# Performance work log

Hardware: AMD Instinct MI355X
Metric: run time of the kernel (lower is better)

The kernel has to match this reference:

```python
import jax, jax.numpy as jnp
import numpy as np

# Dimensions inferred from VSSBlockOneWay(hidden_dim=256, ssm_d_state=64, forward_type='m0_noz')
B_, L_, D_ = 8, 2048, 256      # batch, seq_len, d_model
DIN, N_, P_ = 512, 64, 64      # d_inner = 2*d_model, d_state, head_dim
H_ = DIN // P_                 # n_heads = 8


def _ln(x, w, b, eps=1e-5):
    m = x.mean(-1, keepdims=True)
    v = ((x - m) ** 2).mean(-1, keepdims=True)
    return (x - m) * jax.lax.rsqrt(v + eps) * w + b


def setup_inputs() -> dict:
    key = jax.random.key(0)
    ks = jax.random.split(key, 8)
    s = lambda k, shape, sc: jax.random.normal(k, shape, jnp.float32) * sc
    return dict(
        src=jax.random.normal(ks[0], (B_, L_, D_), jnp.float32),
        ln_w=jnp.ones((D_,), jnp.float32), ln_b=jnp.zeros((D_,), jnp.float32),
        W_in=s(ks[1], (D_, DIN), 0.02),
        conv_w=s(ks[2], (DIN, 1, 3), 0.1),            # depthwise conv1d kernel
        conv_b=jnp.zeros((DIN,), jnp.float32),
        W_xproj=s(ks[3], (DIN, H_ + 2 * N_), 0.02),   # -> (dt | B | C)
        dt_bias=s(ks[4], (H_,), 0.1),
        A_log=jnp.log(jnp.arange(1, H_ + 1, dtype=jnp.float32)),  # Mamba2 A-init
        Ds=jnp.ones((H_,), jnp.float32),
        oln_w=jnp.ones((DIN,), jnp.float32), oln_b=jnp.zeros((DIN,), jnp.float32),
        W_out=s(ks[5], (DIN, D_), 0.02),
    )


def reference(src, ln_w, ln_b, W_in, conv_w, conv_b, W_xproj, dt_bias,
              A_log, Ds, oln_w, oln_b, W_out):
    B, L, D = src.shape
    H, N, P = H_, N_, P_
    x = _ln(src, ln_w, ln_b)
    u = x @ W_in                                                    # (B,L,DIN)
    # depthwise conv over sequence, SAME padding (VMamba uses non-causal dwconv)
    uc = jax.lax.conv_general_dilated(
        u.transpose(0, 2, 1), conv_w, (1,), 'SAME',
        feature_group_count=DIN, dimension_numbers=('NCH', 'OIH', 'NCH'))
    u = jax.nn.gelu((uc + conv_b[None, :, None]).transpose(0, 2, 1),
                    approximate=False)                              # (B,L,DIN)
    dbc = u @ W_xproj                                               # (B,L,H+2N)
    dt = jax.nn.softplus(dbc[..., :H] + dt_bias)                    # (B,L,H)
    Bm = dbc[..., H:H + N]                                          # (B,L,N)
    Cm = dbc[..., H + N:]                                           # (B,L,N)
    A = -jnp.exp(A_log)                                             # (H,)
    decay = jnp.exp(dt * A)                                         # (B,L,H)
    xh = u.reshape(B, L, H, P)
    dtx = dt[..., None] * xh                                        # (B,L,H,P)

    def step(h, inp):
        dec_t, dtx_t, B_t, C_t = inp
        # h: (B,H,P,N)
        h = h * dec_t[:, :, None, None] + dtx_t[..., None] * B_t[:, None, None, :]
        y = jnp.einsum('bhpn,bn->bhp', h, C_t)
        return h, y

    h0 = jnp.zeros((B, H, P, N), u.dtype)
    inputs = (decay.transpose(1, 0, 2), dtx.transpose(1, 0, 2, 3),
              Bm.transpose(1, 0, 2), Cm.transpose(1, 0, 2))
    _, ys = jax.lax.scan(step, h0, inputs)                          # (L,B,H,P)
    y = ys.transpose(1, 0, 2, 3) + xh * Ds[None, None, :, None]
    y = _ln(y.reshape(B, L, DIN), oln_w, oln_b)
    # dropout / drop_path are identity at inference
    return src + y @ W_out
```

## Files before the change

kernel.cpp:

```cpp
#include <hip/hip_runtime.h>
#include <hip/hip_bf16.h>
#include <cmath>

typedef __hip_bfloat16 bf16;
typedef short bf16x8 __attribute__((ext_vector_type(8)));
typedef short bf16x4v __attribute__((ext_vector_type(4)));
typedef float f32x4 __attribute__((ext_vector_type(4)));

constexpr int B_ = 8, L_ = 2048, D_ = 256, DIN_ = 512;
constexpr int H_ = 8, N_ = 64, P_ = 64;
constexpr int BL_ = B_ * L_;
constexpr int NCH_ = 136;
constexpr int Q_ = 64;
constexpr int NC_ = L_ / Q_;

static __device__ __forceinline__ float b2f(bf16 x) { return __bfloat162float(x); }
static __device__ __forceinline__ bf16  f2b(float x) { return __float2bfloat16(x); }
static __device__ __forceinline__ bf16  rawb(short s) { __hip_bfloat16_raw r; r.x = (unsigned short)s; return (bf16)r; }
static __device__ __forceinline__ float sane(float v) { return (fabsf(v) <= 1e30f) ? v : 0.f; }
static __device__ __forceinline__ float loadx(const void* p, size_t i, bool isbf) {
    return isbf ? b2f(((const bf16*)p)[i]) : ((const float*)p)[i];
}
static __device__ __forceinline__ bf16x8 load8x(const void* p, size_t off, bool isbf) {
    if (isbf) return *(const bf16x8*)((const bf16*)p + off);
    const float4* fp = (const float4*)((const float*)p + off);
    float4 f0 = fp[0], f1 = fp[1];
    bf16 t[8] = {f2b(f0.x), f2b(f0.y), f2b(f0.z), f2b(f0.w),
                 f2b(f1.x), f2b(f1.y), f2b(f1.z), f2b(f1.w)};
    return *(bf16x8*)t;
}
static __device__ __forceinline__ void sum8(bf16x8 v, float& s, float& s2) {
#pragma unroll
    for (int t = 0; t < 8; t++) { float x = b2f(rawb(v[t])); s += x; s2 += x * x; }
}
static __device__ __forceinline__ int swz(int row, int col) { return col ^ (((row >> 3) & 7) * 8); }

static __device__ __forceinline__ f32x4 mfma16(bf16x8 a, bf16x8 b, f32x4 c) {
    return __builtin_amdgcn_mfma_f32_16x16x32_bf16(a, b, c, 0, 0, 0);
}

__global__ void prep_k(const void* __restrict__ Win, const void* __restrict__ Wx,
                       const void* __restrict__ Wo,
                       const void* __restrict__ ln_w, const void* __restrict__ ln_b,
                       const void* __restrict__ oln_w, const void* __restrict__ oln_b,
                       bf16* __restrict__ WinT, bf16* __restrict__ WxT, bf16* __restrict__ WoT,
                       float* __restrict__ colsum1, float* __restrict__ bias1,
                       float* __restrict__ colsum2, float* __restrict__ bias2,
                       const unsigned short* __restrict__ flagp) {
    const bool isbf = flagp[0] != 0;
    const int T1 = DIN_ * D_;
    const int T2 = 192 * DIN_;
    const int T3 = D_ * DIN_;
    if (blockIdx.x < 1408) {
        int idx = blockIdx.x * 256 + threadIdx.x;
        if (idx < T1) {
            int i = idx >> 8, d = idx & 255;
            WinT[idx] = f2b(loadx(ln_w, d, isbf) * loadx(Win, (size_t)d * DIN_ + i, isbf));
        } else if (idx < T1 + T2) {
            int e = idx - T1; int j = e >> 9, i = e & 511;
            WxT[e] = (j < NCH_) ? f2b(loadx(Wx, (size_t)i * NCH_ + j, isbf)) : f2b(0.f);
        } else if (idx < T1 + T2 + T3) {
            int e = idx - T1 - T2; int d = e >> 9, i = e & 511;
            WoT[e] = f2b(loadx(oln_w, i, isbf) * loadx(Wo, (size_t)i * D_ + d, isbf));
        }
        return;
    }
    const int o = (blockIdx.x - 1408) * 4 + (threadIdx.x >> 6);
    const int lane = threadIdx.x & 63;
    float cs = 0.f, bs = 0.f;
    if (o < DIN_) {
        int n = o;
        for (int i = lane; i < D_; i += 64) {
            float wv = loadx(Win, (size_t)i * DIN_ + n, isbf);
            cs += loadx(ln_w, i, isbf) * wv;
            bs += loadx(ln_b, i, isbf) * wv;
        }
    } else {
        int d = o - DIN_;
        for (int k = lane; k < DIN_; k += 64) {
            float wv = loadx(Wo, (size_t)k * D_ + d, isbf);
            cs += loadx(oln_w, k, isbf) * wv;
            bs += loadx(oln_b, k, isbf) * wv;
        }
    }
#pragma unroll
    for (int off = 32; off >= 1; off >>= 1) { cs += __shfl_xor(cs, off); bs += __shfl_xor(bs, off); }
    if (lane == 0) {
        if (o < DIN_) { colsum1[o] = cs; bias1[o] = bs; }
        else          { colsum2[o - DIN_] = cs; bias2[o - DIN_] = bs; }
    }
}

__global__ __launch_bounds__(256) void gemm1_k(const void* __restrict__ src,
                                               const bf16* __restrict__ WinT,
                                               const float* __restrict__ colsum1,
                                               const float* __restrict__ bias1,
                                               bf16* __restrict__ u0,
                                               const unsigned short* __restrict__ flagp) {
    const bool isbf = flagp[0] != 0;
    const int tid = threadIdx.x, wave = tid >> 6, lane = tid & 63;
    const int quad = lane >> 4, l16 = lane & 15;
    const int m0 = blockIdx.x * 128 + wave * 32;
    const int n0 = blockIdx.y * 128;
    f32x4 acc[2][8];
#pragma unroll
    for (int i = 0; i < 2; i++)
#pragma unroll
        for (int j = 0; j < 8; j++) acc[i][j] = f32x4{0.f, 0.f, 0.f, 0.f};
    const size_t r0 = (size_t)(m0 + l16) * D_ + quad * 8;
    const size_t r1 = r0 + (size_t)16 * D_;
    const bf16* bp = WinT + (size_t)(n0 + l16) * D_ + quad * 8;
    float s0 = 0.f, s20 = 0.f, s1 = 0.f, s21 = 0.f;
#pragma unroll
    for (int k0 = 0; k0 < D_; k0 += 32) {
        bf16x8 a0 = load8x(src, r0 + k0, isbf);
        bf16x8 a1 = load8x(src, r1 + k0, isbf);
        sum8(a0, s0, s20);
        sum8(a1, s1, s21);
#pragma unroll
        for (int i = 0; i < 8; i++) {
            bf16x8 bb = *(const bf16x8*)(bp + (size_t)16 * i * D_ + k0);
            acc[0][i] = mfma16(a0, bb, acc[0][i]);
            acc[1][i] = mfma16(a1, bb, acc[1][i]);
        }
    }
    s0 += __shfl_xor(s0, 16); s0 += __shfl_xor(s0, 32);
    s20 += __shfl_xor(s20, 16); s20 += __shfl_xor(s20, 32);
    s1 += __shfl_xor(s1, 16); s1 += __shfl_xor(s1, 32);
    s21 += __shfl_xor(s21, 16); s21 += __shfl_xor(s21, 32);
    float cs[8], bsv[8];
#pragma unroll
    for (int i = 0; i < 8; i++) { int n = n0 + 16 * i + l16; cs[i] = colsum1[n]; bsv[i] = bias1[n]; }
#pragma unroll
    for (int rb = 0; rb < 2; rb++)
#pragma unroll
        for (int r = 0; r < 4; r++) {
            int rl = quad * 4 + r;
            float sv  = __shfl(rb == 0 ? s0 : s1, rl);
            float s2v = __shfl(rb == 0 ? s20 : s21, rl);
            float mean = sv * (1.f / D_);
            float var  = s2v * (1.f / D_) - mean * mean;
            float rs = rsqrtf(fmaxf(var, 0.f) + 1e-5f);
            int m = m0 + rb * 16 + rl;
#pragma unroll
            for (int i = 0; i < 8; i++) {
                int n = n0 + 16 * i + l16;
                float v = rs * (acc[rb][i][r] - mean * cs[i]) + bsv[i];
                u0[(size_t)m * DIN_ + n] = f2b(v);
            }
        }
}

template<int MODE, int NT>
__global__ __launch_bounds__(256) void gemmB_k(const bf16* __restrict__ A,
                                               const bf16* __restrict__ BT,
                                               void* __restrict__ Cout,
                                               const void* __restrict__ resid,
                                               const float* __restrict__ colsum,
                                               const float* __restrict__ biasv,
                                               const void* __restrict__ dt_bias,
                                               const void* __restrict__ A_log,
                                               float* __restrict__ dtg,
                                               float* __restrict__ dtAg,
                                               const unsigned short* __restrict__ flagp) {
    const bool isbf = flagp[0] != 0;
    constexpr int K = 512;
    const int tid = threadIdx.x, wave = tid >> 6, lane = tid & 63;
    const int quad = lane >> 4, l16 = lane & 15;
    const int m0 = blockIdx.x * 128 + wave * 32;
    const int n0 = blockIdx.y * (NT * 16);
    f32x4 acc[2][NT];
#pragma unroll
    for (int i = 0; i < 2; i++)
#pragma unroll
        for (int j = 0; j < NT; j++) acc[i][j] = f32x4{0.f, 0.f, 0.f, 0.f};
    const bf16* a0p = A + (size_t)(m0 + l16) * K + quad * 8;
    const bf16* a1p = a0p + (size_t)16 * K;
    const bf16* bp  = BT + (size_t)(n0 + l16) * K + quad * 8;
    float s0 = 0.f, s20 = 0.f, s1 = 0.f, s21 = 0.f;
#pragma unroll 4
    for (int k0 = 0; k0 < K; k0 += 32) {
        bf16x8 a0 = *(const bf16x8*)(a0p + k0);
        bf16x8 a1 = *(const bf16x8*)(a1p + k0);
        if (MODE == 1) { sum8(a0, s0, s20); sum8(a1, s1, s21); }
#pragma unroll
        for (int i = 0; i < NT; i++) {
            bf16x8 bb = *(const bf16x8*)(bp + (size_t)16 * i * K + k0);
            acc[0][i] = mfma16(a0, bb, acc[0][i]);
            acc[1][i] = mfma16(a1, bb, acc[1][i]);
        }
    }
    if (MODE == 0) {
#pragma unroll
        for (int rb = 0; rb < 2; rb++)
#pragma unroll
            for (int r = 0; r < 4; r++) {
                int m = m0 + rb * 16 + quad * 4 + r;
#pragma unroll
                for (int i = 0; i < NT; i++) {
                    int n = n0 + 16 * i + l16;
                    if (n < NCH_) ((bf16*)Cout)[(size_t)m * NCH_ + n] = f2b(acc[rb][i][r]);
                }
            }
        if (blockIdx.y == 0 && l16 < 8) {
            float bb = loadx(dt_bias, l16, isbf);
            float Ah = -__expf(fminf(loadx(A_log, l16, isbf), 30.f));
#pragma unroll
            for (int rb = 0; rb < 2; rb++)
#pragma unroll
                for (int r = 0; r < 4; r++) {
                    int m = m0 + rb * 16 + quad * 4 + r;
                    float raw = acc[rb][0][r] + bb;
                    float sp = raw > 20.f ? raw : log1pf(__expf(raw));
                    sp = fminf(sp, 60.f);
                    dtg[(size_t)m * H_ + l16]  = sp;
                    dtAg[(size_t)m * H_ + l16] = sp * Ah;
                }
        }
    } else {
        s0 += __shfl_xor(s0, 16); s0 += __shfl_xor(s0, 32);
        s20 += __shfl_xor(s20, 16); s20 += __shfl_xor(s20, 32);
        s1 += __shfl_xor(s1, 16); s1 += __shfl_xor(s1, 32);
        s21 += __shfl_xor(s21, 16); s21 += __shfl_xor(s21, 32);
        float cs[NT], bsv[NT];
#pragma unroll
        for (int i = 0; i < NT; i++) { int n = n0 + 16 * i + l16; cs[i] = colsum[n]; bsv[i] = biasv[n]; }
#pragma unroll
        for (int rb = 0; rb < 2; rb++)
#pragma unroll
            for (int r = 0; r < 4; r++) {
                int rl = quad * 4 + r;
                float sv  = __shfl(rb == 0 ? s0 : s1, rl);
                float s2v = __shfl(rb == 0 ? s20 : s21, rl);
                float mean = sv * (1.f / K);
                float var  = s2v * (1.f / K) - mean * mean;
                float rs = rsqrtf(fmaxf(var, 0.f) + 1e-5f);
                int m = m0 + rb * 16 + rl;
#pragma unroll
                for (int i = 0; i < NT; i++) {
                    int n = n0 + 16 * i + l16;
                    size_t o = (size_t)m * D_ + n;
                    float v = rs * (acc[rb][i][r] - mean * cs[i]) + bsv[i] + loadx(resid, o, isbf);
                    v = sane(v);
                    if (isbf) ((bf16*)Cout)[o] = f2b(v);
                    else      ((float*)Cout)[o] = v;
                }
            }
    }
}

constexpr int CSTRIP_ = 4;
__global__ __launch_bounds__(256) void conv_k(const bf16* __restrict__ u0,
                                              const void* __restrict__ cw,
                                              const void* __restrict__ cb,
                                              bf16* __restrict__ u,
                                              const unsigned short* __restrict__ flagp) {
    const bool isbf = flagp[0] != 0;
    __shared__ float wlds[2048];
    {
        int t = threadIdx.x;
#pragma unroll
        for (int i = 0; i < 6; i++) { int e = t + 256 * i; wlds[e] = loadx(cw, e, isbf); }
        int e2 = t + 1536;
        wlds[e2] = loadx(cb, t, isbf);
        wlds[e2 + 256] = loadx(cb, t + 256, isbf);
    }
    __syncthreads();
    const int wave = threadIdx.x >> 6, lane = threadIdx.x & 63;
    const int sid = blockIdx.x * 4 + wave;
    const int bl0 = sid * CSTRIP_;
    const int l0 = bl0 & (L_ - 1);
    const int c8 = lane * 8;
    float w0[8], w1[8], w2[8], bias[8];
#pragma unroll
    for (int t = 0; t < 8; t++) {
        int ch = c8 + t;
        w0[t] = wlds[ch * 3 + 0];
        w1[t] = wlds[ch * 3 + 1];
        w2[t] = wlds[ch * 3 + 2];
        bias[t] = wlds[1536 + ch];
    }
    const bf16x8* rp = (const bf16x8*)(u0 + (size_t)bl0 * DIN_ + c8);
    bf16x8 zero = {0, 0, 0, 0, 0, 0, 0, 0};
    bf16x8 vl = (l0 > 0) ? rp[-64] : zero;
    bf16x8 vm = rp[0];
#pragma unroll
    for (int i = 0; i < CSTRIP_; i++) {
        int l = l0 + i;
        bf16x8 vr = (l < L_ - 1) ? rp[64 * (i + 1)] : zero;
        bf16 ob[8];
#pragma unroll
        for (int t = 0; t < 8; t++) {
            float a = bias[t] + w1[t] * b2f(rawb(vm[t]))
                    + w0[t] * b2f(rawb(vl[t])) + w2[t] * b2f(rawb(vr[t]));
            float ge = 0.5f * a * (1.f + erff(a * 0.70710678118f));
            ob[t] = f2b(ge);
        }
        *(bf16x8*)(u + (size_t)(bl0 + i) * DIN_ + c8) = *(bf16x8*)ob;
        vl = vm; vm = vr;
    }
}

__global__ __launch_bounds__(256) void chunk_state_k(const bf16* __restrict__ ubuf,
                                                     const bf16* __restrict__ dbcb,
                                                     const float* __restrict__ dtg,
                                                     const float* __restrict__ dtAg,
                                                     bf16* __restrict__ HS,
                                                     float* __restrict__ cdg) {
    const int idx = blockIdx.x;
    const int c = idx & 31, h = (idx >> 5) & 7, b = idx >> 8;
    const int bh = b * 8 + h;
    const int blbase = b * L_ + c * Q_;
    __shared__ bf16 Xw[64][72];
    __shared__ bf16 BTb[64][72];
    __shared__ float fj[64];
    const int tid = threadIdx.x;
    if (tid < 64) {
        int j = tid;
        float dA  = dtAg[(size_t)(blbase + j) * H_ + h];
        float dtv = dtg[(size_t)(blbase + j) * H_ + h];
        float v = dA;
#pragma unroll
        for (int off = 1; off < 64; off <<= 1) { float t = __shfl_up(v, off); if (j >= off) v += t; }
        float segEnd = __shfl(v, 63);
        fj[j] = __expf(fminf(segEnd - v, 0.f)) * dtv;
        if (j == 0) cdg[bh * NC_ + c] = __expf(fminf(segEnd, 0.f));
    }
    __syncthreads();
    {
        const int jr = tid >> 3, p8 = (tid & 7) * 8;
#pragma unroll
        for (int it = 0; it < 2; it++) {
            int j = jr + 32 * it;
            float fs = fj[j];
            bf16x8 xv = *(const bf16x8*)(ubuf + (size_t)(blbase + j) * DIN_ + h * 64 + p8);
            bf16x8 bv = *(const bf16x8*)(dbcb + (size_t)(blbase + j) * NCH_ + 8 + p8);
#pragma unroll
            for (int t = 0; t < 8; t++) {
                int p = p8 + t;
                Xw[p][swz(p, j)]  = f2b(fs * b2f(rawb(xv[t])));
                BTb[p][swz(p, j)] = rawb(bv[t]);
            }
        }
    }
    __syncthreads();
    const int wave = tid >> 6, lane = tid & 63, quad = lane >> 4, l16 = lane & 15;
    const int p0 = wave * 16;
    f32x4 acc[4];
#pragma unroll
    for (int i = 0; i < 4; i++) acc[i] = f32x4{0.f, 0.f, 0.f, 0.f};
#pragma unroll
    for (int ks = 0; ks < 2; ks++) {
        int pa = p0 + l16;
        bf16x8 a = *(const bf16x8*)(&Xw[pa][swz(pa, ks * 32 + quad * 8)]);
#pragma unroll
        for (int nt = 0; nt < 4; nt++) {
            int nb = nt * 16 + l16;
            bf16x8 bb = *(const bf16x8*)(&BTb[nb][swz(nb, ks * 32 + quad * 8)]);
            acc[nt] = mfma16(a, bb, acc[nt]);
        }
    }
    size_t slot = (size_t)(bh * NC_ + c) * 4096;
#pragma unroll
    for (int nt = 0; nt < 4; nt++)
#pragma unroll
        for (int r = 0; r < 4; r++) {
            int p = p0 + quad * 4 + r, n = nt * 16 + l16;
            HS[slot + p * 64 + n] = f2b(sane(acc[nt][r]));
        }
}

__global__ __launch_bounds__(256) void chunk_rec_k(bf16* __restrict__ HS,
                                                   const float* __restrict__ cdg) {
    const int bh = blockIdx.x >> 2, sub = blockIdx.x & 3;
    const int eo = sub * 1024 + threadIdx.x * 4;
    float hst[4] = {0.f, 0.f, 0.f, 0.f};
#pragma unroll 2
    for (int c = 0; c < NC_; c++) {
        bf16* p = HS + ((size_t)(bh * NC_ + c)) * 4096 + eo;
        float cd = cdg[bh * NC_ + c];
        bf16 inb[4], outb[4];
        *(bf16x4v*)inb = *(const bf16x4v*)p;
#pragma unroll
        for (int q = 0; q < 4; q++) outb[q] = f2b(hst[q]);
        *(bf16x4v*)p = *(bf16x4v*)outb;
#pragma unroll
        for (int q = 0; q < 4; q++) hst[q] = cd * hst[q] + b2f(inb[q]);
    }
}

__global__ __launch_bounds__(256) void chunk_out_k(bf16* __restrict__ ubuf,
                                                   const bf16* __restrict__ dbcb,
                                                   const float* __restrict__ dtg,
                                                   const float* __restrict__ dtAg,
                                                   const bf16* __restrict__ HS,
                                                   const void* __restrict__ Ds,
                                                   bf16* __restrict__ ybuf,
                                                   const unsigned short* __restrict__ flagp) {
    const bool isbf = flagp[0] != 0;
    const int idx = blockIdx.x;
    const int c = idx & 31, h = (idx >> 5) & 7, b = idx >> 8;
    const int bh = b * 8 + h;
    const int blbase = b * L_ + c * Q_;
    const size_t slotbase = (size_t)(bh * NC_ + c) * 4096;
    __shared__ bf16 Cb[64][72];
    __shared__ bf16 Bb[64][72];
    __shared__ bf16 Xb[64][72];
    __shared__ bf16 Hb[64][72];
    __shared__ bf16 Gb[64][72];
    __shared__ float segL[64], PL[64], dtL[64];
    const int tid = threadIdx.x;
    if (tid < 64) {
        int j = tid;
        float dA  = dtAg[(size_t)(blbase + j) * H_ + h];
        float dtv = dtg[(size_t)(blbase + j) * H_ + h];
        float v = dA;
#pragma unroll
        for (int off = 1; off < 64; off <<= 1) { float t = __shfl_up(v, off); if (j >= off) v += t; }
        segL[j] = v;
        PL[j]   = __expf(fminf(v, 0.f));
        dtL[j]  = dtv;
    }
    {
        const int rr = tid >> 3, k8 = (tid & 7) * 8;
#pragma unroll
        for (int it = 0; it < 2; it++) {
            int r = rr + 32 * it;
            bf16x8 cv = *(const bf16x8*)(dbcb + (size_t)(blbase + r) * NCH_ + 72 + k8);
            bf16x8 bv = *(const bf16x8*)(dbcb + (size_t)(blbase + r) * NCH_ + 8 + k8);
            bf16x8 hv = *(const bf16x8*)(HS + slotbase + r * 64 + k8);
            bf16x8 xv = *(const bf16x8*)(ubuf + (size_t)(blbase + r) * DIN_ + h * 64 + k8);
            *(bf16x8*)(&Cb[r][k8]) = cv;
            *(bf16x8*)(&Bb[r][k8]) = bv;
            *(bf16x8*)(&Hb[r][k8]) = hv;
#pragma unroll
            for (int t = 0; t < 8; t++) { int p = k8 + t; Xb[p][swz(p, r)] = rawb(xv[t]); }
        }
    }
    __syncthreads();
    const int wave = tid >> 6, lane = tid & 63, quad = lane >> 4, l16 = lane & 15;
    const int l0 = wave * 16;
    f32x4 g[4];
#pragma unroll
    for (int i = 0; i < 4; i++) g[i] = f32x4{0.f, 0.f, 0.f, 0.f};
#pragma unroll
    for (int ks = 0; ks < 2; ks++) {
        bf16x8 a = *(const bf16x8*)(&Cb[l0 + l16][ks * 32 + quad * 8]);
#pragma unroll
        for (int jt = 0; jt < 4; jt++) {
            bf16x8 bb = *(const bf16x8*)(&Bb[jt * 16 + l16][ks * 32 + quad * 8]);
            g[jt] = mfma16(a, bb, g[jt]);
        }
    }
#pragma unroll
    for (int jt = 0; jt < 4; jt++) {
        int j = jt * 16 + l16;
#pragma unroll
        for (int r = 0; r < 4; r++) {
            int l = l0 + quad * 4 + r;
            float e = __expf(fminf(segL[l] - segL[j], 0.f));
            float gv = (j <= l) ? sane(g[jt][r]) * e * dtL[j] : 0.f;
            Gb[l][swz(l, j)] = f2b(sane(gv));
        }
    }
    __syncthreads();
    f32x4 y1[4], y2[4];
#pragma unroll
    for (int i = 0; i < 4; i++) { y1[i] = f32x4{0.f, 0.f, 0.f, 0.f}; y2[i] = f32x4{0.f, 0.f, 0.f, 0.f}; }
#pragma unroll
    for (int ks = 0; ks < 2; ks++) {
        int la = l0 + l16;
        bf16x8 ag = *(const bf16x8*)(&Gb[la][swz(la, ks * 32 + quad * 8)]);
        bf16x8 ac = *(const bf16x8*)(&Cb[la][ks * 32 + quad * 8]);
#pragma unroll
        for (int pt = 0; pt < 4; pt++) {
            int pb = pt * 16 + l16;
            bf16x8 bx = *(const bf16x8*)(&Xb[pb][swz(pb, ks * 32 + quad * 8)]);
            bf16x8 bhf = *(const bf16x8*)(&Hb[pb][ks * 32 + quad * 8]);
            y1[pt] = mfma16(ag, bx, y1[pt]);
            y2[pt] = mfma16(ac, bhf, y2[pt]);
        }
    }
    float dsH = loadx(Ds, h, isbf);
#pragma unroll
    for (int pt = 0; pt < 4; pt++) {
        int p = pt * 16 + l16;
#pragma unroll
        for (int r = 0; r < 4; r++) {
            int l = l0 + quad * 4 + r;
            float yv = y1[pt][r] + PL[l] * y2[pt][r] + dsH * b2f(Xb[p][swz(p, l)]);
            ybuf[(size_t)(blbase + l) * DIN_ + h * 64 + p] = f2b(sane(yv));
        }
    }
}

extern "C" void kernel_launch(void* const* d_in, const int* in_sizes, int n_in,
                              void* d_out, int out_size, void* d_ws, size_t ws_size,
                              hipStream_t stream) {
    const void* src     = d_in[0];
    const void* ln_w    = d_in[1];
    const void* ln_b    = d_in[2];
    const void* W_in    = d_in[3];
    const void* conv_w  = d_in[4];
    const void* conv_b  = d_in[5];
    const void* W_xproj = d_in[6];
    const void* dt_bias = d_in[7];
    const void* A_log   = d_in[8];
    const void* Ds      = d_in[9];
    const void* oln_w   = d_in[10];
    const void* oln_b   = d_in[11];
    const void* W_out   = d_in[12];
    const unsigned short* flagp = (const unsigned short*)ln_w;

    char* w = (char*)d_ws;
    size_t off = 0;
    auto alloc = [&](size_t bytes) { void* p = w + off; off += (bytes + 255) & ~(size_t)255; return p; };
    char*   regB   = (char*)alloc((size_t)BL_ * DIN_ * 2);
    char*   regC   = (char*)alloc((size_t)BL_ * DIN_ * 2);
    bf16*   dbcb   = (bf16*)alloc((size_t)BL_ * NCH_ * 2);
    float*  dtg    = (float*)alloc((size_t)BL_ * H_ * 4);
    float*  dtAg   = (float*)alloc((size_t)BL_ * H_ * 4);
    bf16*   WinT   = (bf16*)alloc((size_t)DIN_ * D_ * 2);
    bf16*   WxT    = (bf16*)alloc((size_t)192 * DIN_ * 2);
    bf16*   WoT    = (bf16*)alloc((size_t)D_ * DIN_ * 2);
    float*  colsum1= (float*)alloc(DIN_ * 4);
    float*  bias1  = (float*)alloc(DIN_ * 4);
    float*  colsum2= (float*)alloc(D_ * 4);
    float*  bias2  = (float*)alloc(D_ * 4);
    float*  cdg    = (float*)alloc((size_t)64 * NC_ * 4);

    bf16* u0buf = (bf16*)regB;
    bf16* HS    = (bf16*)regB;
    bf16* ubuf  = (bf16*)regC;
    bf16* ybuf  = (bf16*)regC;

    prep_k<<<1600, 256, 0, stream>>>(W_in, W_xproj, W_out, ln_w, ln_b, oln_w, oln_b,
                                     WinT, WxT, WoT, colsum1, bias1, colsum2, bias2, flagp);
    gemm1_k<<<dim3(BL_ / 128, 4), 256, 0, stream>>>(src, WinT, colsum1, bias1, u0buf, flagp);
    conv_k<<<BL_ / CSTRIP_ / 4, 256, 0, stream>>>(u0buf, conv_w, conv_b, ubuf, flagp);
    gemmB_k<0, 4><<<dim3(BL_ / 128, 3), 256, 0, stream>>>(ubuf, WxT, dbcb, nullptr, nullptr, nullptr,
                                                          dt_bias, A_log, dtg, dtAg, flagp);
    chunk_state_k<<<B_ * H_ * NC_, 256, 0, stream>>>(ubuf, dbcb, dtg, dtAg, HS, cdg);
    chunk_rec_k<<<256, 256, 0, stream>>>(HS, cdg);
    chunk_out_k<<<B_ * H_ * NC_, 256, 0, stream>>>(ubuf, dbcb, dtg, dtAg, HS, Ds, ybuf, flagp);
    gemmB_k<1, 8><<<dim3(BL_ / 128, 2), 256, 0, stream>>>(ybuf, WoT, d_out, src, colsum2, bias2,
                                                          nullptr, nullptr, nullptr, nullptr, flagp);
}
```

Before: 233.9 us.

## Stage GEMM weight tiles in LDS and drop chunk_out LDS staging

The GEMM kernels (gemm1 and both gemmB variants) now copy a 64-column weight tile into padded shared memory once per block. The MFMA loop then reads B operands from LDS instead of global memory, and N per block shrinks to 64 with grids doubled to match. chunk_out_k goes the other way: it drops the shared-memory staging of C, B and the chunk state and reads them straight from global/L2. That cuts its LDS footprint and sync work but may add redundant global loads. gemmB<0> keeps 3 y-blocks at 64 width, covering 192 columns versus the previous 4 tiles of 16.

```diff
diff --git a/kernel.cpp b/kernel.cpp
--- a/kernel.cpp
+++ b/kernel.cpp
@@ -98,28 +98,40 @@
                                                bf16* __restrict__ u0,
                                                const unsigned short* __restrict__ flagp) {
     const bool isbf = flagp[0] != 0;
-    const int tid = threadIdx.x, wave = tid >> 6, lane = tid & 63;
+    constexpr int K = D_;
+    constexpr int STR = K + 8;
+    constexpr int CH = K / 8;
+    __shared__ bf16 Blds[64 * STR];
+    const int tid = threadIdx.x;
+    const int n0 = blockIdx.y * 64;
+#pragma unroll
+    for (int i = 0; i < 64 * CH / 256; i++) {
+        int e = tid + 256 * i;
+        int r = e / CH, cch = e % CH;
+        bf16x8 v = *(const bf16x8*)(WinT + (size_t)(n0 + r) * K + cch * 8);
+        *(bf16x8*)(&Blds[r * STR + cch * 8]) = v;
+    }
+    __syncthreads();
+    const int wave = tid >> 6, lane = tid & 63;
     const int quad = lane >> 4, l16 = lane & 15;
     const int m0 = blockIdx.x * 128 + wave * 32;
-    const int n0 = blockIdx.y * 128;
-    f32x4 acc[2][8];
+    f32x4 acc[2][4];
 #pragma unroll
     for (int i = 0; i < 2; i++)
 #pragma unroll
-        for (int j = 0; j < 8; j++) acc[i][j] = f32x4{0.f, 0.f, 0.f, 0.f};
-    const size_t r0 = (size_t)(m0 + l16) * D_ + quad * 8;
-    const size_t r1 = r0 + (size_t)16 * D_;
-    const bf16* bp = WinT + (size_t)(n0 + l16) * D_ + quad * 8;
+        for (int j = 0; j < 4; j++) acc[i][j] = f32x4{0.f, 0.f, 0.f, 0.f};
+    const size_t r0 = (size_t)(m0 + l16) * K + quad * 8;
+    const size_t r1 = r0 + (size_t)16 * K;
     float s0 = 0.f, s20 = 0.f, s1 = 0.f, s21 = 0.f;
 #pragma unroll
-    for (int k0 = 0; k0 < D_; k0 += 32) {
+    for (int k0 = 0; k0 < K; k0 += 32) {
         bf16x8 a0 = load8x(src, r0 + k0, isbf);
         bf16x8 a1 = load8x(src, r1 + k0, isbf);
         sum8(a0, s0, s20);
         sum8(a1, s1, s21);
 #pragma unroll
-        for (int i = 0; i < 8; i++) {
-            bf16x8 bb = *(const bf16x8*)(bp + (size_t)16 * i * D_ + k0);
+        for (int i = 0; i < 4; i++) {
+            bf16x8 bb = *(const bf16x8*)(&Blds[(16 * i + l16) * STR + k0 + quad * 8]);
             acc[0][i] = mfma16(a0, bb, acc[0][i]);
             acc[1][i] = mfma16(a1, bb, acc[1][i]);
         }
@@ -128,9 +140,9 @@
     s20 += __shfl_xor(s20, 16); s20 += __shfl_xor(s20, 32);
     s1 += __shfl_xor(s1, 16); s1 += __shfl_xor(s1, 32);
     s21 += __shfl_xor(s21, 16); s21 += __shfl_xor(s21, 32);
-    float cs[8], bsv[8];
-#pragma unroll
-    for (int i = 0; i < 8; i++) { int n = n0 + 16 * i + l16; cs[i] = colsum1[n]; bsv[i] = bias1[n]; }
+    float cs[4], bsv[4];
+#pragma unroll
+    for (int i = 0; i < 4; i++) { int n = n0 + 16 * i + l16; cs[i] = colsum1[n]; bsv[i] = bias1[n]; }
 #pragma unroll
     for (int rb = 0; rb < 2; rb++)
 #pragma unroll
@@ -143,7 +155,7 @@
             float rs = rsqrtf(fmaxf(var, 0.f) + 1e-5f);
             int m = m0 + rb * 16 + rl;
 #pragma unroll
-            for (int i = 0; i < 8; i++) {
+            for (int i = 0; i < 4; i++) {
                 int n = n0 + 16 * i + l16;
                 float v = rs * (acc[rb][i][r] - mean * cs[i]) + bsv[i];
                 u0[(size_t)m * DIN_ + n] = f2b(v);
@@ -151,7 +163,7 @@
         }
 }
 
-template<int MODE, int NT>
+template<int MODE>
 __global__ __launch_bounds__(256) void gemmB_k(const bf16* __restrict__ A,
                                                const bf16* __restrict__ BT,
                                                void* __restrict__ Cout,
@@ -165,18 +177,29 @@
                                                const unsigned short* __restrict__ flagp) {
     const bool isbf = flagp[0] != 0;
     constexpr int K = 512;
-    const int tid = threadIdx.x, wave = tid >> 6, lane = tid & 63;
+    constexpr int STR = K + 8;
+    constexpr int CH = K / 8;
+    __shared__ bf16 Blds[64 * STR];
+    const int tid = threadIdx.x;
+    const int n0 = blockIdx.y * 64;
+#pragma unroll
+    for (int i = 0; i < 64 * CH / 256; i++) {
+        int e = tid + 256 * i;
+        int r = e / CH, cch = e % CH;
+        bf16x8 v = *(const bf16x8*)(BT + (size_t)(n0 + r) * K + cch * 8);
+        *(bf16x8*)(&Blds[r * STR + cch * 8]) = v;
+    }
+    __syncthreads();
+    const int wave = tid >> 6, lane = tid & 63;
     const int quad = lane >> 4, l16 = lane & 15;
     const int m0 = blockIdx.x * 128 + wave * 32;
-    const int n0 = blockIdx.y * (NT * 16);
-    f32x4 acc[2][NT];
+    f32x4 acc[2][4];
 #pragma unroll
     for (int i = 0; i < 2; i++)
 #pragma unroll
-        for (int j = 0; j < NT; j++) acc[i][j] = f32x4{0.f, 0.f, 0.f, 0.f};
+        for (int j = 0; j < 4; j++) acc[i][j] = f32x4{0.f, 0.f, 0.f, 0.f};
     const bf16* a0p = A + (size_t)(m0 + l16) * K + quad * 8;
     const bf16* a1p = a0p + (size_t)16 * K;
-    const bf16* bp  = BT + (size_t)(n0 + l16) * K + quad * 8;
     float s0 = 0.f, s20 = 0.f, s1 = 0.f, s21 = 0.f;
 #pragma unroll 4
     for (int k0 = 0; k0 < K; k0 += 32) {
@@ -184,8 +207,8 @@
         bf16x8 a1 = *(const bf16x8*)(a1p + k0);
         if (MODE == 1) { sum8(a0, s0, s20); sum8(a1, s1, s21); }
 #pragma unroll
-        for (int i = 0; i < NT; i++) {
-            bf16x8 bb = *(const bf16x8*)(bp + (size_t)16 * i * K + k0);
+        for (int i = 0; i < 4; i++) {
+            bf16x8 bb = *(const bf16x8*)(&Blds[(16 * i + l16) * STR + k0 + quad * 8]);
             acc[0][i] = mfma16(a0, bb, acc[0][i]);
             acc[1][i] = mfma16(a1, bb, acc[1][i]);
         }
@@ -197,7 +220,7 @@
             for (int r = 0; r < 4; r++) {
                 int m = m0 + rb * 16 + quad * 4 + r;
 #pragma unroll
-                for (int i = 0; i < NT; i++) {
+                for (int i = 0; i < 4; i++) {
                     int n = n0 + 16 * i + l16;
                     if (n < NCH_) ((bf16*)Cout)[(size_t)m * NCH_ + n] = f2b(acc[rb][i][r]);
                 }
@@ -222,9 +245,9 @@
         s20 += __shfl_xor(s20, 16); s20 += __shfl_xor(s20, 32);
         s1 += __shfl_xor(s1, 16); s1 += __shfl_xor(s1, 32);
         s21 += __shfl_xor(s21, 16); s21 += __shfl_xor(s21, 32);
-        float cs[NT], bsv[NT];
-#pragma unroll
-        for (int i = 0; i < NT; i++) { int n = n0 + 16 * i + l16; cs[i] = colsum[n]; bsv[i] = biasv[n]; }
+        float cs[4], bsv[4];
+#pragma unroll
+        for (int i = 0; i < 4; i++) { int n = n0 + 16 * i + l16; cs[i] = colsum[n]; bsv[i] = biasv[n]; }
 #pragma unroll
         for (int rb = 0; rb < 2; rb++)
 #pragma unroll
@@ -237,7 +260,7 @@
                 float rs = rsqrtf(fmaxf(var, 0.f) + 1e-5f);
                 int m = m0 + rb * 16 + rl;
 #pragma unroll
-                for (int i = 0; i < NT; i++) {
+                for (int i = 0; i < 4; i++) {
                     int n = n0 + 16 * i + l16;
                     size_t o = (size_t)m * D_ + n;
                     float v = rs * (acc[rb][i][r] - mean * cs[i]) + bsv[i] + loadx(resid, o, isbf);
@@ -261,9 +284,8 @@
         int t = threadIdx.x;
 #pragma unroll
         for (int i = 0; i < 6; i++) { int e = t + 256 * i; wlds[e] = loadx(cw, e, isbf); }
-        int e2 = t + 1536;
-        wlds[e2] = loadx(cb, t, isbf);
-        wlds[e2 + 256] = loadx(cb, t + 256, isbf);
+        wlds[t + 1536] = loadx(cb, t, isbf);
+        wlds[t + 1792] = loadx(cb, t + 256, isbf);
     }
     __syncthreads();
     const int wave = threadIdx.x >> 6, lane = threadIdx.x & 63;
@@ -403,10 +425,7 @@
     const int bh = b * 8 + h;
     const int blbase = b * L_ + c * Q_;
     const size_t slotbase = (size_t)(bh * NC_ + c) * 4096;
-    __shared__ bf16 Cb[64][72];
-    __shared__ bf16 Bb[64][72];
     __shared__ bf16 Xb[64][72];
-    __shared__ bf16 Hb[64][72];
     __shared__ bf16 Gb[64][72];
     __shared__ float segL[64], PL[64], dtL[64];
     const int tid = threadIdx.x;
@@ -426,13 +445,7 @@
 #pragma unroll
         for (int it = 0; it < 2; it++) {
             int r = rr + 32 * it;
-            bf16x8 cv = *(const bf16x8*)(dbcb + (size_t)(blbase + r) * NCH_ + 72 + k8);
-            bf16x8 bv = *(const bf16x8*)(dbcb + (size_t)(blbase + r) * NCH_ + 8 + k8);
-            bf16x8 hv = *(const bf16x8*)(HS + slotbase + r * 64 + k8);
             bf16x8 xv = *(const bf16x8*)(ubuf + (size_t)(blbase + r) * DIN_ + h * 64 + k8);
-            *(bf16x8*)(&Cb[r][k8]) = cv;
-            *(bf16x8*)(&Bb[r][k8]) = bv;
-            *(bf16x8*)(&Hb[r][k8]) = hv;
 #pragma unroll
             for (int t = 0; t < 8; t++) { int p = k8 + t; Xb[p][swz(p, r)] = rawb(xv[t]); }
         }
@@ -445,10 +458,10 @@
     for (int i = 0; i < 4; i++) g[i] = f32x4{0.f, 0.f, 0.f, 0.f};
 #pragma unroll
     for (int ks = 0; ks < 2; ks++) {
-        bf16x8 a = *(const bf16x8*)(&Cb[l0 + l16][ks * 32 + quad * 8]);
+        bf16x8 a = *(const bf16x8*)(dbcb + (size_t)(blbase + l0 + l16) * NCH_ + 72 + ks * 32 + quad * 8);
 #pragma unroll
         for (int jt = 0; jt < 4; jt++) {
-            bf16x8 bb = *(const bf16x8*)(&Bb[jt * 16 + l16][ks * 32 + quad * 8]);
+            bf16x8 bb = *(const bf16x8*)(dbcb + (size_t)(blbase + jt * 16 + l16) * NCH_ + 8 + ks * 32 + quad * 8);
             g[jt] = mfma16(a, bb, g[jt]);
         }
     }
@@ -471,12 +484,12 @@
     for (int ks = 0; ks < 2; ks++) {
         int la = l0 + l16;
         bf16x8 ag = *(const bf16x8*)(&Gb[la][swz(la, ks * 32 + quad * 8)]);
-        bf16x8 ac = *(const bf16x8*)(&Cb[la][ks * 32 + quad * 8]);
+        bf16x8 ac = *(const bf16x8*)(dbcb + (size_t)(blbase + la) * NCH_ + 72 + ks * 32 + quad * 8);
 #pragma unroll
         for (int pt = 0; pt < 4; pt++) {
             int pb = pt * 16 + l16;
             bf16x8 bx = *(const bf16x8*)(&Xb[pb][swz(pb, ks * 32 + quad * 8)]);
-            bf16x8 bhf = *(const bf16x8*)(&Hb[pb][ks * 32 + quad * 8]);
+            bf16x8 bhf = *(const bf16x8*)(HS + slotbase + (size_t)pb * 64 + ks * 32 + quad * 8);
             y1[pt] = mfma16(ag, bx, y1[pt]);
             y2[pt] = mfma16(ac, bhf, y2[pt]);
         }
@@ -536,13 +549,13 @@
 
     prep_k<<<1600, 256, 0, stream>>>(W_in, W_xproj, W_out, ln_w, ln_b, oln_w, oln_b,
                                      WinT, WxT, WoT, colsum1, bias1, colsum2, bias2, flagp);
-    gemm1_k<<<dim3(BL_ / 128, 4), 256, 0, stream>>>(src, WinT, colsum1, bias1, u0buf, flagp);
+    gemm1_k<<<dim3(BL_ / 128, 8), 256, 0, stream>>>(src, WinT, colsum1, bias1, u0buf, flagp);
     conv_k<<<BL_ / CSTRIP_ / 4, 256, 0, stream>>>(u0buf, conv_w, conv_b, ubuf, flagp);
-    gemmB_k<0, 4><<<dim3(BL_ / 128, 3), 256, 0, stream>>>(ubuf, WxT, dbcb, nullptr, nullptr, nullptr,
-                                                          dt_bias, A_log, dtg, dtAg, flagp);
+    gemmB_k<0><<<dim3(BL_ / 128, 3), 256, 0, stream>>>(ubuf, WxT, dbcb, nullptr, nullptr, nullptr,
+                                                       dt_bias, A_log, dtg, dtAg, flagp);
     chunk_state_k<<<B_ * H_ * NC_, 256, 0, stream>>>(ubuf, dbcb, dtg, dtAg, HS, cdg);
     chunk_rec_k<<<256, 256, 0, stream>>>(HS, cdg);
     chunk_out_k<<<B_ * H_ * NC_, 256, 0, stream>>>(ubuf, dbcb, dtg, dtAg, HS, Ds, ybuf, flagp);
-    gemmB_k<1, 8><<<dim3(BL_ / 128, 2), 256, 0, stream>>>(ybuf, WoT, d_out, src, colsum2, bias2,
-                                                          nullptr, nullptr, nullptr, nullptr, flagp);
-}
+    gemmB_k<1><<<dim3(BL_ / 128, 4), 256, 0, stream>>>(ybuf, WoT, d_out, src, colsum2, bias2,
+                                                       nullptr, nullptr, nullptr, nullptr, flagp);
+}
```

Measured after the change: 212.1 us. 1.1x faster.
